# Optimization experiments

Hardware: AMD Instinct MI355X
Metric: run time of the kernel (lower is better)

The kernel has to match this reference:

```python
import jax, jax.numpy as jnp
import numpy as np
import math

N_QUBITS = 8
N_LAYERS = 4
DIM = 2 ** N_QUBITS


def _ry(theta):
    # theta: (...,) -> (..., 2, 2) real RY matrix, cast to complex64
    c, s = jnp.cos(theta / 2), jnp.sin(theta / 2)
    g = jnp.stack([jnp.stack([c, -s], -1), jnp.stack([s, c], -1)], -2)
    return g.astype(jnp.complex64)


def _apply_1q(psi, gate, q):
    # psi: (B, 2**n); gate: (2,2) shared or (B,2,2) per-sample; qubit q (wire 0 = MSB)
    B = psi.shape[0]
    L, R = 2 ** q, 2 ** (N_QUBITS - q - 1)
    s = psi.reshape(B, L, 2, R)
    if gate.ndim == 2:
        s = jnp.einsum('ij,bljr->blir', gate, s)
    else:
        s = jnp.einsum('bij,bljr->blir', gate, s)
    return s.reshape(B, DIM)


def _cnot(psi, c):
    # CNOT on adjacent wires (c, c+1): swap |10> <-> |11> on that 4-dim block
    B = psi.shape[0]
    L, R = 2 ** c, 2 ** (N_QUBITS - c - 2)
    s = psi.reshape(B, L, 4, R)
    s = s[:, :, jnp.array([0, 1, 3, 2]), :]
    return s.reshape(B, DIM)


def setup_inputs() -> dict:
    key = jax.random.key(0)
    kx, kw = jax.random.split(key)
    B = 65536
    x = jax.random.uniform(kx, (B, N_QUBITS), jnp.float32, -math.pi, math.pi)
    bound = 1.0 / math.sqrt(N_QUBITS)
    weights = jax.random.uniform(kw, (N_LAYERS, N_QUBITS, 2), jnp.float32, -bound, bound)
    return {"x": x, "weights": weights}


def reference(x, weights):
    B = x.shape[0]
    # |0...0> initial state
    psi = jnp.zeros((B, DIM), jnp.complex64).at[:, 0].set(1.0)
    # angle encoding: RY(x_i) on wire i (per-sample gates)
    enc = _ry(x)  # (B, n, 2, 2)
    for q in range(N_QUBITS):
        psi = _apply_1q(psi, enc[:, q], q)
    # variational layers: RY(w[l,i,0]) then RZ(w[l,i,1]) on each wire, then CNOT chain
    for l in range(N_LAYERS):
        ry = _ry(weights[l, :, 0])  # (n, 2, 2)
        tz = weights[l, :, 1]
        ez_m = jnp.exp(-0.5j * tz.astype(jnp.complex64))  # e^{-i theta/2}
        ez_p = jnp.exp(0.5j * tz.astype(jnp.complex64))   # e^{+i theta/2}
        phases = jnp.stack([ez_m, ez_p], axis=-1)  # (n, 2) diag of RZ
        g = phases[:, :, None] * ry  # (n,2,2) = RZ @ RY (fused rotation)
        for q in range(N_QUBITS):
            psi = _apply_1q(psi, g[q], q)
        for c in range(N_QUBITS - 1):
            psi = _cnot(psi, c)
    # PauliZ expectations per wire
    p = psi.real ** 2 + psi.imag ** 2  # (B, DIM)
    exps = []
    for q in range(N_QUBITS):
        pq = p.reshape(B, 2 ** q, 2, -1).sum(axis=(1, 3))  # (B, 2)
        exps.append(pq[:, 0] - pq[:, 1])
    return jnp.stack(exps, axis=1)  # (B, n_qubits)
```

## Files before the change

### kernel.cpp

```cpp
#include <hip/hip_runtime.h>


typedef _Float16 half8  __attribute__((ext_vector_type(8)));
typedef float    float4v __attribute__((ext_vector_type(4)));
typedef unsigned int uint2v __attribute__((ext_vector_type(2)));
typedef unsigned int uint4v __attribute__((ext_vector_type(4)));

#define MEMFENCE() __asm__ volatile("" ::: "memory")

__device__ __forceinline__ unsigned pk2(float a, float b) {
  auto v = __builtin_amdgcn_cvt_pkrtz(a, b);
  return __builtin_bit_cast(unsigned, v);
}
__device__ __forceinline__ float rdlane(float v, int l) {
  return __builtin_bit_cast(float, __builtin_amdgcn_readlane(__builtin_bit_cast(int, v), l));
}
__device__ __forceinline__ unsigned sw8u(unsigned v) {
  return (unsigned)__builtin_amdgcn_mov_dpp((int)v, 0x128, 0xf, 0xf, false);
}
__device__ __forceinline__ float sw8f(float v) {
  return __builtin_bit_cast(float,
      __builtin_amdgcn_mov_dpp(__builtin_bit_cast(int, v), 0x128, 0xf, 0xf, false));
}
__device__ __forceinline__ int tauf(int l) {
  int y = l ^ (((l >> 3) & 1) << 2);
  y ^= ((y >> 2) & 1) << 1;
  y ^= (y >> 1) & 1;
  return y;
}

__launch_bounds__(256, 4)
__global__ void qmain(const float* __restrict__ x, const float* __restrict__ w,
                      float* __restrict__ out) {
  __shared__ __align__(16) unsigned char smem[40960];
  const int tid = threadIdx.x;
  const int lane = tid & 63, wv = tid >> 6;
  const int quad = lane >> 4, n = lane & 15;

  {
    const int t = wv;
    int mr = n ^ ((n >> 1) & 1);
    mr ^= ((mr >> 2) & 1) << 1;
    mr ^= ((mr >> 3) & 1) << 2;
    float cS[8], sS[8], zcS[8], zsS[8];
#pragma unroll
    for (int qq = 0; qq < 8; ++qq) {
      float th = w[(t * 8 + qq) * 2 + 0];
      float tz = w[(t * 8 + qq) * 2 + 1];
      __sincosf(0.5f * th, &sS[qq], &cS[qq]);
      __sincosf(0.5f * tz, &zsS[qq], &zcS[qq]);
    }
    union { _Float16 h[8]; half8 v; } bLR, bLI, bRR, bRI;
#pragma unroll
    for (int ci = 0; ci < 4; ++ci) {
      const int kp = quad * 4 + ci;
      float hr = 1.f, hi = 0.f;
#pragma unroll
      for (int j = 0; j < 4; ++j) {
        int rb = (mr >> (3 - j)) & 1, cb = (kp >> (3 - j)) & 1;
        float ryv = (rb == cb) ? cS[j] : (rb ? sS[j] : -sS[j]);
        float ar = zcS[j] * ryv;
        float ai = (rb ? zsS[j] : -zsS[j]) * ryv;
        float nr = hr * ar - hi * ai, ni = hr * ai + hi * ar;
        hr = nr; hi = ni;
      }
      bLR.h[2 * ci] = (_Float16)hr;  bLR.h[2 * ci + 1] = (_Float16)(-hi);
      bLI.h[2 * ci] = (_Float16)hi;  bLI.h[2 * ci + 1] = (_Float16)hr;
      int yk = tauf(kp);
      float wr = 1.f, wi = 0.f;
#pragma unroll
      for (int j = 0; j < 4; ++j) {
        int rb = (n >> (3 - j)) & 1, cb = (yk >> (3 - j)) & 1;
        float ryv = (rb == cb) ? cS[4 + j] : (rb ? sS[4 + j] : -sS[4 + j]);
        float ar = zcS[4 + j] * ryv;
        float ai = (rb ? zsS[4 + j] : -zsS[4 + j]) * ryv;
        float nr = wr * ar - wi * ai, ni = wr * ai + wi * ar;
        wr = nr; wi = ni;
      }
      bRR.h[2 * ci] = (_Float16)wr;  bRR.h[2 * ci + 1] = (_Float16)(-wi);
      bRI.h[2 * ci] = (_Float16)wi;  bRI.h[2 * ci + 1] = (_Float16)wr;
    }
    half8* FB = (half8*)(smem + 8192);
    FB[(t * 4 + 0) * 64 + lane] = bLR.v;
    FB[(t * 4 + 1) * 64 + lane] = bLI.v;
    FB[(t * 4 + 2) * 64 + lane] = bRR.v;
    FB[(t * 4 + 3) * 64 + lane] = bRI.v;
  }
  __syncthreads();
  half8 BLR[4], BLI[4], BRR[4], BRI[4];
#pragma unroll
  for (int t = 0; t < 4; ++t) {
    const half8* FB = (const half8*)(smem + 8192);
    BLR[t] = FB[(t * 4 + 0) * 64 + lane];
    BLI[t] = FB[(t * 4 + 1) * 64 + lane];
    BRR[t] = FB[(t * 4 + 2) * 64 + lane];
    BRI[t] = FB[(t * 4 + 3) * 64 + lane];
  }
#pragma unroll
  for (int c = 0; c < 8; ++c) {
    union { _Float16 h[8]; half8 v; } sg;
#pragma unroll
    for (int jj = 0; jj < 8; ++jj) {
      int u = (quad & 1) * 8 + jj;
      int y = tauf(2 * c + (quad >> 1));
      float sv = 0.f;
      if (n < 8) {
        int bit = (n < 4) ? ((u >> (3 - n)) & 1) : ((y >> (7 - n)) & 1);
        sv = bit ? -1.f : 1.f;
      }
      sg.h[jj] = (_Float16)sv;
    }
    *(half8*)(smem + c * 1024 + lane * 16) = sg.v;
  }
  __syncthreads();

  unsigned char* smp = smem + 8192 + wv * 8192;
  const unsigned pWg = (unsigned)(2 * n + (quad >> 1));
  const unsigned pWlo = (unsigned)((quad & 1) * 8);
  const int e0 = (blockIdx.x * 4 + wv) * 16;
  const float4v zz = {0.f, 0.f, 0.f, 0.f};
  const int ytau = tauf(n);

  const float* xp = x + (size_t)e0 * 8;
  float xA = xp[lane], xB = xp[64 + lane];
  float CA, SA, CB, SB;
  __sincosf(0.5f * xA, &SA, &CA);
  __sincosf(0.5f * xB, &SB, &CB);

  for (int i = 0; i < 8; ++i) {
    uint4v st[2];
#pragma unroll
    for (int h = 0; h < 2; ++h) {
      const int e = 2 * i + h;
      const float cs = (i < 4) ? CA : CB;
      const float sn = (i < 4) ? SA : SB;
      const int lb = (e & 7) * 8;
      float cq[8], sq[8];
#pragma unroll
      for (int q = 0; q < 8; ++q) { cq[q] = rdlane(cs, lb + q); sq[q] = rdlane(sn, lb + q); }
      float f0 = (quad & 2) ? sq[0] : cq[0];
      float f1 = (quad & 1) ? sq[1] : cq[1];
      float f4 = (ytau & 8) ? sq[4] : cq[4];
      float f5 = (ytau & 4) ? sq[5] : cq[5];
      float f6 = (ytau & 2) ? sq[6] : cq[6];
      float f7 = (ytau & 1) ? sq[7] : cq[7];
      float pb = f0 * f1 * f4 * f5 * f6 * f7;
      st[h][0] = pk2(pb * cq[2] * cq[3], 0.f);
      st[h][1] = pk2(pb * cq[2] * sq[3], 0.f);
      st[h][2] = pk2(pb * sq[2] * cq[3], 0.f);
      st[h][3] = pk2(pb * sq[2] * sq[3], 0.f);
    }

#pragma unroll
    for (int t = 0; t < 4; ++t) {
      float4v xr[2], xi[2];
#pragma unroll
      for (int c = 0; c < 2; ++c) {
        half8 A = __builtin_bit_cast(half8, st[c]);
        xr[c] = __builtin_amdgcn_mfma_f32_16x16x32_f16(A, BLR[t], zz, 0, 0, 0);
        xi[c] = __builtin_amdgcn_mfma_f32_16x16x32_f16(A, BLI[t], zz, 0, 0, 0);
      }
      uint4v X[2];
#pragma unroll
      for (int c = 0; c < 2; ++c) {
        X[c][0] = pk2(xr[c][0], xi[c][0]);
        X[c][1] = pk2(xr[c][1], xi[c][1]);
        X[c][2] = pk2(xr[c][2], xi[c][2]);
        X[c][3] = pk2(xr[c][3], xi[c][3]);
      }
      float4v yr[2], yi[2];
#pragma unroll
      for (int c = 0; c < 2; ++c) {
        half8 XA = __builtin_bit_cast(half8, X[c]);
        yr[c] = __builtin_amdgcn_mfma_f32_16x16x32_f16(XA, BRR[t], zz, 0, 0, 0);
        yi[c] = __builtin_amdgcn_mfma_f32_16x16x32_f16(XA, BRI[t], zz, 0, 0, 0);
      }
      if (t < 3) {
#pragma unroll
        for (int c = 0; c < 2; ++c) {
          st[c][0] = pk2(yr[c][0], yi[c][0]);
          st[c][1] = sw8u(pk2(yr[c][1], yi[c][1]));
          st[c][2] = pk2(yr[c][2], yi[c][2]);
          st[c][3] = sw8u(pk2(yr[c][3], yi[c][3]));
        }
      } else {
        MEMFENCE();
#pragma unroll
        for (int c = 0; c < 2; ++c) {
          float r1 = sw8f(yr[c][1]), i1 = sw8f(yi[c][1]);
          float r3 = sw8f(yr[c][3]), i3 = sw8f(yi[c][3]);
          float p0 = yr[c][0] * yr[c][0] + yi[c][0] * yi[c][0];
          float p1 = r1 * r1 + i1 * i1;
          float p2 = yr[c][2] * yr[c][2] + yi[c][2] * yi[c][2];
          float p3 = r3 * r3 + i3 * i3;
          const unsigned e = (unsigned)(2 * i + c);
          unsigned pOff = e * 512u + ((pWg ^ (e & 7u)) << 4) + pWlo;
          uint2v v = { pk2(p0, p1), pk2(p2, p3) };
          *(uint2v*)(smp + pOff) = v;
        }
        MEMFENCE();
      }
    }
  }

  float4v acc = zz;
  MEMFENCE();
#pragma unroll
  for (int c = 0; c < 8; ++c) {
    half8 sfv = *(const half8*)(smem + c * 1024 + lane * 16);
    unsigned pR = (unsigned)(n * 512 +
                             ((((unsigned)(c * 4 + quad)) ^ (unsigned)(n & 7)) << 4));
    half8 pbv = *(const half8*)(smp + pR);
    acc = __builtin_amdgcn_mfma_f32_16x16x32_f16(sfv, pbv, acc, 0, 0, 0);
  }
  MEMFENCE();
  if (quad < 2) {
    float4v* o = (float4v*)(out + (size_t)(e0 + n) * 8 + quad * 4);
    *o = acc;
  }
}

extern "C" void kernel_launch(void* const* d_in, const int* in_sizes, int n_in,
                              void* d_out, int out_size, void* d_ws, size_t ws_size,
                              hipStream_t stream) {
  const float* x = (const float*)d_in[0];
  const float* w = (const float*)d_in[1];
  float* out = (float*)d_out;
  qmain<<<dim3(1024), dim3(256), 0, stream>>>(x, w, out);
}
```

Measured before the change: 80.52 us.

## Stage encoding sin/cos in LDS, keep sign matrix in registers, disable outer unroll

Replaces the 16 readlane broadcasts per sample, which go through scalar registers, with a per-wave LDS table of cos/sin pairs read back as float4 vectors. The constant sign matrix used for the final Pauli-Z reduction now stays in registers instead of LDS, and the shared-memory layout is compacted, cutting LDS use from 40 KB to 36 KB per block. The outer sample loop is explicitly kept rolled to limit code size and register pressure. In exchange it adds an extra barrier, more LDS reads in the hot loop, and 8 more half8 registers held live.

```diff
diff --git a/kernel.cpp b/kernel.cpp
--- a/kernel.cpp
+++ b/kernel.cpp
@@ -3,6 +3,7 @@
 
 typedef _Float16 half8  __attribute__((ext_vector_type(8)));
 typedef float    float4v __attribute__((ext_vector_type(4)));
+typedef float    float2v __attribute__((ext_vector_type(2)));
 typedef unsigned int uint2v __attribute__((ext_vector_type(2)));
 typedef unsigned int uint4v __attribute__((ext_vector_type(4)));
 
@@ -11,9 +12,6 @@
 __device__ __forceinline__ unsigned pk2(float a, float b) {
   auto v = __builtin_amdgcn_cvt_pkrtz(a, b);
   return __builtin_bit_cast(unsigned, v);
-}
-__device__ __forceinline__ float rdlane(float v, int l) {
-  return __builtin_bit_cast(float, __builtin_amdgcn_readlane(__builtin_bit_cast(int, v), l));
 }
 __device__ __forceinline__ unsigned sw8u(unsigned v) {
   return (unsigned)__builtin_amdgcn_mov_dpp((int)v, 0x128, 0xf, 0xf, false);
@@ -32,7 +30,7 @@
 __launch_bounds__(256, 4)
 __global__ void qmain(const float* __restrict__ x, const float* __restrict__ w,
                       float* __restrict__ out) {
-  __shared__ __align__(16) unsigned char smem[40960];
+  __shared__ __align__(16) unsigned char smem[36864];
   const int tid = threadIdx.x;
   const int lane = tid & 63, wv = tid >> 6;
   const int quad = lane >> 4, n = lane & 15;
@@ -80,7 +78,7 @@
       bRR.h[2 * ci] = (_Float16)wr;  bRR.h[2 * ci + 1] = (_Float16)(-wi);
       bRI.h[2 * ci] = (_Float16)wi;  bRI.h[2 * ci + 1] = (_Float16)wr;
     }
-    half8* FB = (half8*)(smem + 8192);
+    half8* FB = (half8*)smem;
     FB[(t * 4 + 0) * 64 + lane] = bLR.v;
     FB[(t * 4 + 1) * 64 + lane] = bLI.v;
     FB[(t * 4 + 2) * 64 + lane] = bRR.v;
@@ -90,12 +88,15 @@
   half8 BLR[4], BLI[4], BRR[4], BRI[4];
 #pragma unroll
   for (int t = 0; t < 4; ++t) {
-    const half8* FB = (const half8*)(smem + 8192);
+    const half8* FB = (const half8*)smem;
     BLR[t] = FB[(t * 4 + 0) * 64 + lane];
     BLI[t] = FB[(t * 4 + 1) * 64 + lane];
     BRR[t] = FB[(t * 4 + 2) * 64 + lane];
     BRI[t] = FB[(t * 4 + 3) * 64 + lane];
   }
+  __syncthreads();
+
+  half8 sf[8];
 #pragma unroll
   for (int c = 0; c < 8; ++c) {
     union { _Float16 h[8]; half8 v; } sg;
@@ -110,45 +111,52 @@
       }
       sg.h[jj] = (_Float16)sv;
     }
-    *(half8*)(smem + c * 1024 + lane * 16) = sg.v;
-  }
-  __syncthreads();
-
-  unsigned char* smp = smem + 8192 + wv * 8192;
+    sf[c] = sg.v;
+  }
+
+  unsigned char* smp = smem + wv * 8192;
+  unsigned char* cst = smem + 32768 + wv * 1024;
   const unsigned pWg = (unsigned)(2 * n + (quad >> 1));
   const unsigned pWlo = (unsigned)((quad & 1) * 8);
   const int e0 = (blockIdx.x * 4 + wv) * 16;
   const float4v zz = {0.f, 0.f, 0.f, 0.f};
   const int ytau = tauf(n);
 
-  const float* xp = x + (size_t)e0 * 8;
-  float xA = xp[lane], xB = xp[64 + lane];
-  float CA, SA, CB, SB;
-  __sincosf(0.5f * xA, &SA, &CA);
-  __sincosf(0.5f * xB, &SB, &CB);
-
+  {
+    const float* xp = x + (size_t)e0 * 8;
+    float xa = xp[lane], xb = xp[64 + lane];
+    float CA, SA, CB, SB;
+    __sincosf(0.5f * xa, &SA, &CA);
+    __sincosf(0.5f * xb, &SB, &CB);
+    MEMFENCE();
+    *(float2v*)(cst + lane * 8) = (float2v){CA, SA};
+    *(float2v*)(cst + 512 + lane * 8) = (float2v){CB, SB};
+    MEMFENCE();
+  }
+
+#pragma clang loop unroll(disable)
   for (int i = 0; i < 8; ++i) {
     uint4v st[2];
 #pragma unroll
     for (int h = 0; h < 2; ++h) {
-      const int e = 2 * i + h;
-      const float cs = (i < 4) ? CA : CB;
-      const float sn = (i < 4) ? SA : SB;
-      const int lb = (e & 7) * 8;
-      float cq[8], sq[8];
-#pragma unroll
-      for (int q = 0; q < 8; ++q) { cq[q] = rdlane(cs, lb + q); sq[q] = rdlane(sn, lb + q); }
-      float f0 = (quad & 2) ? sq[0] : cq[0];
-      float f1 = (quad & 1) ? sq[1] : cq[1];
-      float f4 = (ytau & 8) ? sq[4] : cq[4];
-      float f5 = (ytau & 4) ? sq[5] : cq[5];
-      float f6 = (ytau & 2) ? sq[6] : cq[6];
-      float f7 = (ytau & 1) ? sq[7] : cq[7];
+      const unsigned ctoff = (unsigned)(2 * i + h) * 64u;
+      float4v t01 = *(const float4v*)(cst + ctoff);
+      float4v t23 = *(const float4v*)(cst + ctoff + 16);
+      float4v t45 = *(const float4v*)(cst + ctoff + 32);
+      float4v t67 = *(const float4v*)(cst + ctoff + 48);
+      float f0 = (quad & 2) ? t01[1] : t01[0];
+      float f1 = (quad & 1) ? t01[3] : t01[2];
+      float f4 = (ytau & 8) ? t45[1] : t45[0];
+      float f5 = (ytau & 4) ? t45[3] : t45[2];
+      float f6 = (ytau & 2) ? t67[1] : t67[0];
+      float f7 = (ytau & 1) ? t67[3] : t67[2];
       float pb = f0 * f1 * f4 * f5 * f6 * f7;
-      st[h][0] = pk2(pb * cq[2] * cq[3], 0.f);
-      st[h][1] = pk2(pb * cq[2] * sq[3], 0.f);
-      st[h][2] = pk2(pb * sq[2] * cq[3], 0.f);
-      st[h][3] = pk2(pb * sq[2] * sq[3], 0.f);
+      float cc = t23[0] * t23[2], cs = t23[0] * t23[3];
+      float sc = t23[1] * t23[2], ss = t23[1] * t23[3];
+      st[h][0] = pk2(pb * cc, 0.f);
+      st[h][1] = pk2(pb * cs, 0.f);
+      st[h][2] = pk2(pb * sc, 0.f);
+      st[h][3] = pk2(pb * ss, 0.f);
     }
 
 #pragma unroll
@@ -207,11 +215,10 @@
   MEMFENCE();
 #pragma unroll
   for (int c = 0; c < 8; ++c) {
-    half8 sfv = *(const half8*)(smem + c * 1024 + lane * 16);
     unsigned pR = (unsigned)(n * 512 +
                              ((((unsigned)(c * 4 + quad)) ^ (unsigned)(n & 7)) << 4));
     half8 pbv = *(const half8*)(smp + pR);
-    acc = __builtin_amdgcn_mfma_f32_16x16x32_f16(sfv, pbv, acc, 0, 0, 0);
+    acc = __builtin_amdgcn_mfma_f32_16x16x32_f16(sf[c], pbv, acc, 0, 0, 0);
   }
   MEMFENCE();
   if (quad < 2) {
```

Result: slower. 83.82 us (+4.1%).
